# Optimization experiments

Measured on AMD Instinct MI355X. Metric: run time of the kernel, lower is better.

## Reference

```python
import jax, jax.numpy as jnp
import numpy as np

B, N, C = 2, 2048, 1024
H = 16
D = C // H  # head_dim = 64
SCALE = D ** -0.5


def setup_inputs() -> dict:
    key = jax.random.key(0)
    ks = jax.random.split(key, 9)
    s = C ** -0.5  # ~ torch Linear default init scale
    return {
        "x": jax.random.normal(ks[0], (B, N, C), dtype=jnp.float32),
        "Wq": jax.random.uniform(ks[1], (C, C), jnp.float32, -s, s),
        "bq": jax.random.uniform(ks[2], (C,), jnp.float32, -s, s),
        "Wk": jax.random.uniform(ks[3], (C, C), jnp.float32, -s, s),
        "bk": jax.random.uniform(ks[4], (C,), jnp.float32, -s, s),
        "Wv": jax.random.uniform(ks[5], (C, C), jnp.float32, -s, s),
        "bv": jax.random.uniform(ks[6], (C,), jnp.float32, -s, s),
        "Wo": jax.random.uniform(ks[7], (C, C), jnp.float32, -s, s),
        "bo": jax.random.uniform(ks[8], (C,), jnp.float32, -s, s),
    }


def reference(x, Wq, bq, Wk, bk, Wv, bv, Wo, bo):
    # Projections: [B,N,C] -> [B,H,N,D]
    def split_heads(t):
        return t.reshape(B, N, H, D).transpose(0, 2, 1, 3)

    q = split_heads(x @ Wq.T + bq)
    k = split_heads(x @ Wk.T + bk)
    v = split_heads(x @ Wv.T + bv)

    scores = jnp.einsum("bhnd,bhmd->bhnm", q, k) * SCALE  # [B,H,N,N]
    attn = jax.nn.softmax(scores, axis=-1)
    out = jnp.einsum("bhnm,bhmd->bhnd", attn, v)  # [B,H,N,D]
    out = out.transpose(0, 2, 1, 3).reshape(B, N, C)
    return out @ Wo.T + bo
```

## Files before the change

### kernel.cpp

```cpp
#include <hip/hip_runtime.h>
#include <stdint.h>


typedef _Float16 h8 __attribute__((ext_vector_type(8)));
typedef _Float16 h4 __attribute__((ext_vector_type(4)));
typedef float f4 __attribute__((ext_vector_type(4)));
typedef float f16f __attribute__((ext_vector_type(16)));
typedef uint32_t u32;
typedef u32 u32x4 __attribute__((ext_vector_type(4)));

#define AS1(p) ((const __attribute__((address_space(1))) void*)(p))
#define AS3(p) ((__attribute__((address_space(3))) void*)(p))

template <int ITERS>
__device__ __forceinline__ void stage128B(const _Float16* g, int ldk, _Float16* s, int tid) {
#pragma unroll
  for (int j = 0; j < ITERS; ++j) {
    int off = j * 4096 + tid * 16;
    int row = off >> 7;
    int ch = (off >> 4) & 7;
    int gch = ch ^ (row & 7);
    __builtin_amdgcn_global_load_lds(AS1(g + row * ldk + gch * 8), AS3(s + (off >> 1)), 16, 0, 0);
  }
}

__device__ __forceinline__ void stage_vt(const _Float16* g, _Float16* s, int tid) {
#pragma unroll
  for (int j = 0; j < 4; ++j) {
    int off = j * 4096 + tid * 16;
    int row = off >> 8;
    int ch = (off >> 4) & 15;
    int gch = ch ^ (row & 15);
    __builtin_amdgcn_global_load_lds(AS1(g + row * 2048 + gch * 8), AS3(s + (off >> 1)), 16, 0, 0);
  }
}

__device__ __forceinline__ h8 frag64(const _Float16* s, int row, int g) {
  return *(const h8*)(s + row * 64 + ((g ^ (row & 7)) << 3));
}

__global__ void cvt_all(const float* __restrict__ x, const float* __restrict__ Wq,
                        const float* __restrict__ Wk, const float* __restrict__ Wv,
                        const float* __restrict__ Wo, _Float16* __restrict__ xh,
                        _Float16* __restrict__ q, _Float16* __restrict__ k,
                        _Float16* __restrict__ v, _Float16* __restrict__ o) {
  int blk = blockIdx.x;
  const float* src; _Float16* dst; int off;
  if (blk < 4096)      { src = x;  dst = xh; off = blk; }
  else if (blk < 5120) { src = Wq; dst = q;  off = blk - 4096; }
  else if (blk < 6144) { src = Wk; dst = k;  off = blk - 5120; }
  else if (blk < 7168) { src = Wv; dst = v;  off = blk - 6144; }
  else                 { src = Wo; dst = o;  off = blk - 7168; }
  int i = off * 1024 + threadIdx.x * 4;
  f4 vv = *(const f4*)(src + i);
  h4 ov;
  ov[0] = (_Float16)vv[0]; ov[1] = (_Float16)vv[1]; ov[2] = (_Float16)vv[2]; ov[3] = (_Float16)vv[3];
  *(h4*)(dst + i) = ov;
}

__global__ __launch_bounds__(256, 3) void gemm_qkv(
    const _Float16* __restrict__ X,
    const _Float16* __restrict__ W0, const _Float16* __restrict__ W1, const _Float16* __restrict__ W2,
    const float* __restrict__ b0, const float* __restrict__ b1, const float* __restrict__ b2,
    _Float16* __restrict__ O0, _Float16* __restrict__ O1, _Float16* __restrict__ O2) {
  __shared__ _Float16 As[128 * 64];
  __shared__ _Float16 Bs[128 * 64];
  int z = blockIdx.z;
  const _Float16* W = (z == 0) ? W0 : (z == 1) ? W1 : W2;
  const float* bias = (z == 0) ? b0 : (z == 1) ? b1 : b2;

  int tid = threadIdx.x;
  int lane = tid & 63, wave = tid >> 6;
  int quad = lane >> 4, l15 = lane & 15;
  int wm = (wave >> 1) << 6, wn = (wave & 1) << 6;
  int m0 = blockIdx.y << 7, n0 = blockIdx.x << 7;

  f4 acc[4][4] = {};
  for (int k0 = 0; k0 < 1024; k0 += 64) {
    stage128B<4>(X + m0 * 1024 + k0, 1024, As, tid);
    stage128B<4>(W + n0 * 1024 + k0, 1024, Bs, tid);
    __syncthreads();
#pragma unroll
    for (int ks = 0; ks < 2; ++ks) {
      h8 af[4], bf[4];
#pragma unroll
      for (int i = 0; i < 4; ++i) af[i] = frag64(As, wm + i * 16 + l15, ks * 4 + quad);
#pragma unroll
      for (int i = 0; i < 4; ++i) bf[i] = frag64(Bs, wn + i * 16 + l15, ks * 4 + quad);
#pragma unroll
      for (int mi = 0; mi < 4; ++mi)
#pragma unroll
        for (int ni = 0; ni < 4; ++ni)
          acc[mi][ni] = __builtin_amdgcn_mfma_f32_16x16x32_f16(af[mi], bf[ni], acc[mi][ni], 0, 0, 0);
    }
    __syncthreads();
  }

  if (z == 2) {
#pragma unroll
    for (int mi = 0; mi < 4; ++mi) {
#pragma unroll
      for (int ni = 0; ni < 4; ++ni) {
        int o = n0 + wn + ni * 16 + l15;
        float bv = bias[o];
        int h = o >> 6, dd = o & 63;
        int m = m0 + wm + mi * 16 + quad * 4;
        int b = m >> 11, n = m & 2047;
        h4 v;
#pragma unroll
        for (int r = 0; r < 4; ++r) v[r] = (_Float16)(acc[mi][ni][r] + bv);
        *(h4*)(O2 + (((b * 16 + h) * 64 + dd) * 2048 + n)) = v;
      }
    }
  } else {
    float scale = (z == 0) ? 0.125f * 1.44269504089f : 1.0f;
    _Float16* Out = (z == 0) ? O0 : O1;
#pragma unroll
    for (int mi = 0; mi < 4; ++mi) {
#pragma unroll
      for (int ni = 0; ni < 4; ++ni) {
        int o = n0 + wn + ni * 16 + l15;
        float bv = bias[o];
        int h = o >> 6, d = o & 63;
#pragma unroll
        for (int r = 0; r < 4; ++r) {
          int m = m0 + wm + mi * 16 + quad * 4 + r;
          int b = m >> 11, n = m & 2047;
          float v = (acc[mi][ni][r] + bv) * scale;
          Out[(((b * 16 + h) * 2048 + n) << 6) + d] = (_Float16)v;
        }
      }
    }
  }
}

__global__ __launch_bounds__(256, 3) void gemm_out(
    const _Float16* __restrict__ A, const _Float16* __restrict__ W,
    const float* __restrict__ bias, float* __restrict__ Out) {
  __shared__ _Float16 As[128 * 64];
  __shared__ _Float16 Bs[64 * 64];
  int tid = threadIdx.x;
  int lane = tid & 63, wave = tid >> 6;
  int quad = lane >> 4, l15 = lane & 15;
  int wm = (wave >> 1) << 6, wn = (wave & 1) << 5;
  int m0 = blockIdx.y << 7, n0 = blockIdx.x << 6;

  f4 acc[4][2] = {};
  for (int k0 = 0; k0 < 1024; k0 += 64) {
    stage128B<4>(A + m0 * 1024 + k0, 1024, As, tid);
    stage128B<2>(W + n0 * 1024 + k0, 1024, Bs, tid);
    __syncthreads();
#pragma unroll
    for (int ks = 0; ks < 2; ++ks) {
      h8 af[4], bf[2];
#pragma unroll
      for (int i = 0; i < 4; ++i) af[i] = frag64(As, wm + i * 16 + l15, ks * 4 + quad);
#pragma unroll
      for (int i = 0; i < 2; ++i) bf[i] = frag64(Bs, wn + i * 16 + l15, ks * 4 + quad);
#pragma unroll
      for (int mi = 0; mi < 4; ++mi)
#pragma unroll
        for (int ni = 0; ni < 2; ++ni)
          acc[mi][ni] = __builtin_amdgcn_mfma_f32_16x16x32_f16(af[mi], bf[ni], acc[mi][ni], 0, 0, 0);
    }
    __syncthreads();
  }
#pragma unroll
  for (int mi = 0; mi < 4; ++mi) {
#pragma unroll
    for (int ni = 0; ni < 2; ++ni) {
      int o = n0 + wn + ni * 16 + l15;
      float bv = bias[o];
#pragma unroll
      for (int r = 0; r < 4; ++r) {
        int m = m0 + wm + mi * 16 + quad * 4 + r;
        Out[m * 1024 + o] = acc[mi][ni][r] + bv;
      }
    }
  }
}

__global__ __launch_bounds__(256, 2) void attn(
    const _Float16* __restrict__ Q, const _Float16* __restrict__ Kv,
    const _Float16* __restrict__ Vt, _Float16* __restrict__ AO) {
  __shared__ _Float16 Ks[2][128 * 64];
  __shared__ _Float16 Vs[2][64 * 128];
  int tid = threadIdx.x, lane = tid & 63, wave = tid >> 6;
  int h = lane >> 5, l31 = lane & 31;
  int bh = blockIdx.y, q0 = blockIdx.x << 7;

  const _Float16* Qb = Q + (bh * 2048 + q0 + wave * 32 + l31) * 64;
  h8 qf[4];
#pragma unroll
  for (int ks4 = 0; ks4 < 4; ++ks4)
    qf[ks4] = *(const h8*)(Qb + ks4 * 16 + h * 8);

  int krow = (l31 & 19) | ((l31 & 4) << 1) | ((l31 & 8) >> 1);
  int kch = krow & 7;
  int vch = l31 & 15;

  const _Float16* Kb = Kv + bh * 131072;
  const _Float16* Vb = Vt + bh * 131072;
  f16f oacc[2] = {};
  float lsum = 0.f;

  stage128B<4>(Kb, 64, Ks[0], tid);
  stage_vt(Vb, Vs[0], tid);

  for (int kt = 0; kt < 16; ++kt) {
    int cur = kt & 1;
    __syncthreads();
    if (kt < 15) {
      stage128B<4>(Kb + (kt + 1) * 8192, 64, Ks[cur ^ 1], tid);
      stage_vt(Vb + (kt + 1) * 128, Vs[cur ^ 1], tid);
    }
    const _Float16* Kst = Ks[cur];
    const _Float16* Vst = Vs[cur];

    f16f sacc[4] = {};
#pragma unroll
    for (int ks4 = 0; ks4 < 4; ++ks4) {
      int pch = ((ks4 * 2 + h) ^ kch) << 3;
#pragma unroll
      for (int kt2 = 0; kt2 < 4; ++kt2) {
        h8 kf = *(const h8*)(Kst + kt2 * 2048 + krow * 64 + pch);
        sacc[kt2] = __builtin_amdgcn_mfma_f32_32x32x16_f16(kf, qf[ks4], sacc[kt2], 0, 0, 0);
      }
    }

    u32 pkw[4][8];
#pragma unroll
    for (int g = 0; g < 4; ++g) {
#pragma unroll
      for (int i = 0; i < 8; ++i) {
        float pa = __builtin_amdgcn_exp2f(sacc[g][2 * i]);
        float pb = __builtin_amdgcn_exp2f(sacc[g][2 * i + 1]);
        lsum += pa + pb;
        pkw[g][i] = __builtin_bit_cast(u32, __builtin_amdgcn_cvt_pkrtz(pa, pb));
      }
    }

#pragma unroll
    for (int g = 0; g < 4; ++g) {
#pragma unroll
      for (int s = 0; s < 2; ++s) {
        u32x4 pw = {pkw[g][4 * s], pkw[g][4 * s + 1], pkw[g][4 * s + 2], pkw[g][4 * s + 3]};
        h8 pb = __builtin_bit_cast(h8, pw);
        int ch = ((g * 4 + s * 2 + h) ^ vch) << 3;
#pragma unroll
        for (int dt = 0; dt < 2; ++dt) {
          h8 vf = *(const h8*)(Vst + (dt * 32 + l31) * 128 + ch);
          oacc[dt] = __builtin_amdgcn_mfma_f32_32x32x16_f16(vf, pb, oacc[dt], 0, 0, 0);
        }
      }
    }
  }

  float l = lsum + __shfl_xor(lsum, 32);
  float inv = 1.0f / l;
  int b = bh >> 4, hh = bh & 15;
  int n = q0 + wave * 32 + l31;
  _Float16* base = AO + (b * 2048 + n) * 1024 + hh * 64;
#pragma unroll
  for (int dt = 0; dt < 2; ++dt) {
#pragma unroll
    for (int b2 = 0; b2 < 4; ++b2) {
      h4 o;
#pragma unroll
      for (int a = 0; a < 4; ++a) o[a] = (_Float16)(oacc[dt][b2 * 4 + a] * inv);
      *(h4*)(base + dt * 32 + b2 * 8 + h * 4) = o;
    }
  }
}

extern "C" void kernel_launch(void* const* d_in, const int* in_sizes, int n_in,
                              void* d_out, int out_size, void* d_ws, size_t ws_size,
                              hipStream_t stream) {
  const float* x = (const float*)d_in[0];
  const float* Wq = (const float*)d_in[1];
  const float* bq = (const float*)d_in[2];
  const float* Wk = (const float*)d_in[3];
  const float* bk = (const float*)d_in[4];
  const float* Wv = (const float*)d_in[5];
  const float* bv = (const float*)d_in[6];
  const float* Wo = (const float*)d_in[7];
  const float* bo = (const float*)d_in[8];
  float* out = (float*)d_out;

  char* w = (char*)d_ws;
  _Float16* xh  = (_Float16*)(w);
  _Float16* Wqh = (_Float16*)(w + (8u << 20));
  _Float16* Wkh = (_Float16*)(w + (10u << 20));
  _Float16* Wvh = (_Float16*)(w + (12u << 20));
  _Float16* Woh = (_Float16*)(w + (14u << 20));
  _Float16* Qh  = (_Float16*)(w + (16u << 20));
  _Float16* Kh  = (_Float16*)(w + (24u << 20));
  _Float16* Vth = (_Float16*)(w + (32u << 20));
  _Float16* AOh = xh;

  cvt_all<<<8192, 256, 0, stream>>>(x, Wq, Wk, Wv, Wo, xh, Wqh, Wkh, Wvh, Woh);
  gemm_qkv<<<dim3(8, 32, 3), 256, 0, stream>>>(xh, Wqh, Wkh, Wvh, bq, bk, bv, Qh, Kh, Vth);
  attn<<<dim3(16, 32), 256, 0, stream>>>(Qh, Kh, Vth, AOh);
  gemm_out<<<dim3(16, 32), 256, 0, stream>>>(AOh, Woh, bo, out);
}
```

Measured before the change: 176.1 us.

## Split attention key range across wave pairs with triple-buffered 64-key stages

The attention kernel now runs 512 threads per block. Each pair of waves shares 32 query rows and splits every 64-key tile, with each wave taking 32 keys. Staging moves from double-buffered 128-key tiles to triple-buffered 64-key tiles, so the kernel has smaller per-wave register state and more waves in flight to hide latency. At the end, partial outputs and row sums are reduced through shared memory, which adds an extra sync and LDS traffic. The softmax still has no max subtraction, the same as before.

```diff
diff --git a/kernel.cpp b/kernel.cpp
--- a/kernel.cpp
+++ b/kernel.cpp
@@ -24,15 +24,12 @@
   }
 }
 
-__device__ __forceinline__ void stage_vt(const _Float16* g, _Float16* s, int tid) {
-#pragma unroll
-  for (int j = 0; j < 4; ++j) {
-    int off = j * 4096 + tid * 16;
-    int row = off >> 8;
-    int ch = (off >> 4) & 15;
-    int gch = ch ^ (row & 15);
-    __builtin_amdgcn_global_load_lds(AS1(g + row * 2048 + gch * 8), AS3(s + (off >> 1)), 16, 0, 0);
-  }
+__device__ __forceinline__ void stage8k(const _Float16* g, int ldk, _Float16* s, int tid) {
+  int off = tid * 16;
+  int row = off >> 7;
+  int ch = (off >> 4) & 7;
+  int gch = ch ^ (row & 7);
+  __builtin_amdgcn_global_load_lds(AS1(g + row * ldk + gch * 8), AS3(s + (off >> 1)), 16, 0, 0);
 }
 
 __device__ __forceinline__ h8 frag64(const _Float16* s, int row, int g) {
@@ -180,95 +177,114 @@
   }
 }
 
-__global__ __launch_bounds__(256, 2) void attn(
+__global__ __launch_bounds__(512, 4) void attn(
     const _Float16* __restrict__ Q, const _Float16* __restrict__ Kv,
     const _Float16* __restrict__ Vt, _Float16* __restrict__ AO) {
-  __shared__ _Float16 Ks[2][128 * 64];
-  __shared__ _Float16 Vs[2][64 * 128];
+  __shared__ _Float16 smem[6 * 4096];
+  _Float16* Ksb = smem;
+  _Float16* Vsb = smem + 3 * 4096;
+
   int tid = threadIdx.x, lane = tid & 63, wave = tid >> 6;
   int h = lane >> 5, l31 = lane & 31;
+  int p = wave & 1, qg = wave >> 1;
   int bh = blockIdx.y, q0 = blockIdx.x << 7;
 
-  const _Float16* Qb = Q + (bh * 2048 + q0 + wave * 32 + l31) * 64;
+  const _Float16* Qb = Q + (bh * 2048 + q0 + qg * 32 + l31) * 64;
   h8 qf[4];
 #pragma unroll
   for (int ks4 = 0; ks4 < 4; ++ks4)
     qf[ks4] = *(const h8*)(Qb + ks4 * 16 + h * 8);
 
   int krow = (l31 & 19) | ((l31 & 4) << 1) | ((l31 & 8) >> 1);
-  int kch = krow & 7;
-  int vch = l31 & 15;
+  int kbase = (p * 32 + krow) * 64;
+  int kx = krow & 7;
+  int vx = l31 & 7;
 
   const _Float16* Kb = Kv + bh * 131072;
   const _Float16* Vb = Vt + bh * 131072;
   f16f oacc[2] = {};
   float lsum = 0.f;
 
-  stage128B<4>(Kb, 64, Ks[0], tid);
-  stage_vt(Vb, Vs[0], tid);
-
-  for (int kt = 0; kt < 16; ++kt) {
-    int cur = kt & 1;
-    __syncthreads();
-    if (kt < 15) {
-      stage128B<4>(Kb + (kt + 1) * 8192, 64, Ks[cur ^ 1], tid);
-      stage_vt(Vb + (kt + 1) * 128, Vs[cur ^ 1], tid);
-    }
-    const _Float16* Kst = Ks[cur];
-    const _Float16* Vst = Vs[cur];
-
-    f16f sacc[4] = {};
+  stage8k(Kb, 64, Ksb, tid);
+  stage8k(Vb, 2048, Vsb, tid);
+  stage8k(Kb + 4096, 64, Ksb + 4096, tid);
+  stage8k(Vb + 64, 2048, Vsb + 4096, tid);
+
+  int bp = 0;
+  for (int ph = 0; ph < 32; ++ph) {
+    __syncthreads();
+    if (ph < 30) {
+      int sl = bp ? bp - 1 : 2;
+      int pr = ph + 2;
+      stage8k(Kb + pr * 4096, 64, Ksb + sl * 4096, tid);
+      stage8k(Vb + pr * 64, 2048, Vsb + sl * 4096, tid);
+    }
+    const _Float16* Kst = Ksb + bp * 4096;
+    const _Float16* Vst = Vsb + bp * 4096;
+
+    f16f sacc = {};
 #pragma unroll
     for (int ks4 = 0; ks4 < 4; ++ks4) {
-      int pch = ((ks4 * 2 + h) ^ kch) << 3;
-#pragma unroll
-      for (int kt2 = 0; kt2 < 4; ++kt2) {
-        h8 kf = *(const h8*)(Kst + kt2 * 2048 + krow * 64 + pch);
-        sacc[kt2] = __builtin_amdgcn_mfma_f32_32x32x16_f16(kf, qf[ks4], sacc[kt2], 0, 0, 0);
-      }
-    }
-
-    u32 pkw[4][8];
-#pragma unroll
-    for (int g = 0; g < 4; ++g) {
-#pragma unroll
-      for (int i = 0; i < 8; ++i) {
-        float pa = __builtin_amdgcn_exp2f(sacc[g][2 * i]);
-        float pb = __builtin_amdgcn_exp2f(sacc[g][2 * i + 1]);
-        lsum += pa + pb;
-        pkw[g][i] = __builtin_bit_cast(u32, __builtin_amdgcn_cvt_pkrtz(pa, pb));
-      }
-    }
-
-#pragma unroll
-    for (int g = 0; g < 4; ++g) {
-#pragma unroll
-      for (int s = 0; s < 2; ++s) {
-        u32x4 pw = {pkw[g][4 * s], pkw[g][4 * s + 1], pkw[g][4 * s + 2], pkw[g][4 * s + 3]};
-        h8 pb = __builtin_bit_cast(h8, pw);
-        int ch = ((g * 4 + s * 2 + h) ^ vch) << 3;
-#pragma unroll
-        for (int dt = 0; dt < 2; ++dt) {
-          h8 vf = *(const h8*)(Vst + (dt * 32 + l31) * 128 + ch);
-          oacc[dt] = __builtin_amdgcn_mfma_f32_32x32x16_f16(vf, pb, oacc[dt], 0, 0, 0);
-        }
-      }
-    }
-  }
-
-  float l = lsum + __shfl_xor(lsum, 32);
-  float inv = 1.0f / l;
-  int b = bh >> 4, hh = bh & 15;
-  int n = q0 + wave * 32 + l31;
-  _Float16* base = AO + (b * 2048 + n) * 1024 + hh * 64;
-#pragma unroll
-  for (int dt = 0; dt < 2; ++dt) {
-#pragma unroll
-    for (int b2 = 0; b2 < 4; ++b2) {
-      h4 o;
-#pragma unroll
-      for (int a = 0; a < 4; ++a) o[a] = (_Float16)(oacc[dt][b2 * 4 + a] * inv);
-      *(h4*)(base + dt * 32 + b2 * 8 + h * 4) = o;
+      h8 kf = *(const h8*)(Kst + kbase + (((ks4 * 2 + h) ^ kx) << 3));
+      sacc = __builtin_amdgcn_mfma_f32_32x32x16_f16(kf, qf[ks4], sacc, 0, 0, 0);
+    }
+
+    u32 pkw[8];
+#pragma unroll
+    for (int i = 0; i < 8; ++i) {
+      float pa = __builtin_amdgcn_exp2f(sacc[2 * i]);
+      float pb = __builtin_amdgcn_exp2f(sacc[2 * i + 1]);
+      lsum += pa + pb;
+      pkw[i] = __builtin_bit_cast(u32, __builtin_amdgcn_cvt_pkrtz(pa, pb));
+    }
+
+#pragma unroll
+    for (int s = 0; s < 2; ++s) {
+      u32x4 pw = {pkw[4 * s], pkw[4 * s + 1], pkw[4 * s + 2], pkw[4 * s + 3]};
+      h8 pb = __builtin_bit_cast(h8, pw);
+      int ch = (((p << 2) | (s << 1) | h) ^ vx) << 3;
+#pragma unroll
+      for (int dt = 0; dt < 2; ++dt) {
+        h8 vf = *(const h8*)(Vst + (dt * 32 + l31) * 64 + ch);
+        oacc[dt] = __builtin_amdgcn_mfma_f32_32x32x16_f16(vf, pb, oacc[dt], 0, 0, 0);
+      }
+    }
+    bp = (bp == 2) ? 0 : bp + 1;
+  }
+
+  __syncthreads();
+  float* cb = (float*)smem;
+  if (p) {
+    float* w = cb + (qg * 64 + lane) * 33;
+#pragma unroll
+    for (int i = 0; i < 16; ++i) w[i] = oacc[0][i];
+#pragma unroll
+    for (int i = 0; i < 16; ++i) w[16 + i] = oacc[1][i];
+    w[32] = lsum;
+  }
+  __syncthreads();
+  if (!p) {
+    const float* r = cb + (qg * 64 + lane) * 33;
+#pragma unroll
+    for (int i = 0; i < 16; ++i) oacc[0][i] += r[i];
+#pragma unroll
+    for (int i = 0; i < 16; ++i) oacc[1][i] += r[16 + i];
+    lsum += r[32];
+
+    float l = lsum + __shfl_xor(lsum, 32);
+    float inv = 1.0f / l;
+    int b = bh >> 4, hh = bh & 15;
+    int n = q0 + qg * 32 + l31;
+    _Float16* base = AO + (b * 2048 + n) * 1024 + hh * 64;
+#pragma unroll
+    for (int dt = 0; dt < 2; ++dt) {
+#pragma unroll
+      for (int b2 = 0; b2 < 4; ++b2) {
+        h4 o;
+#pragma unroll
+        for (int a = 0; a < 4; ++a) o[a] = (_Float16)(oacc[dt][b2 * 4 + a] * inv);
+        *(h4*)(base + dt * 32 + b2 * 8 + h * 4) = o;
+      }
     }
   }
 }
@@ -300,6 +316,6 @@
 
   cvt_all<<<8192, 256, 0, stream>>>(x, Wq, Wk, Wv, Wo, xh, Wqh, Wkh, Wvh, Woh);
   gemm_qkv<<<dim3(8, 32, 3), 256, 0, stream>>>(xh, Wqh, Wkh, Wvh, bq, bk, bv, Qh, Kh, Vth);
-  attn<<<dim3(16, 32), 256, 0, stream>>>(Qh, Kh, Vth, AOh);
+  attn<<<dim3(16, 32), 512, 0, stream>>>(Qh, Kh, Vth, AOh);
   gemm_out<<<dim3(16, 32), 256, 0, stream>>>(AOh, Woh, bo, out);
 }
```

After: 183.9 us. 1.04x slower.
